# Kernel optimization log

Hardware: AMD Instinct MI355X
Metric: run time of the kernel (lower is better)

## Reference

```python
import jax, jax.numpy as jnp
import numpy as np
from jax import lax

D_MODEL = 1024
D_STATE = 16
D_CONV = 4
EXPAND = 2
D_INNER = EXPAND * D_MODEL
LN_EPS = 1e-5


def setup_inputs() -> dict:
    key = jax.random.key(0)
    ks = jax.random.split(key, 12)
    B, L = 4, 1024
    s = lambda fan_in: 1.0 / np.sqrt(fan_in)
    inp = {
        "x": jax.random.normal(ks[0], (B, L, D_MODEL), jnp.float32),
        # in_proj: d_model -> 2*d_inner (stored as (in, out))
        "W_in": jax.random.normal(ks[1], (D_MODEL, 2 * D_INNER), jnp.float32) * s(D_MODEL),
        "b_in": jnp.zeros((2 * D_INNER,), jnp.float32),
        # depthwise causal conv1d, kernel (d_inner, 1, d_conv)
        "conv_w": jax.random.normal(ks[2], (D_INNER, 1, D_CONV), jnp.float32) * s(D_CONV),
        "conv_b": jnp.zeros((D_INNER,), jnp.float32),
        # x_proj: d_inner -> 2*d_state
        "W_xp": jax.random.normal(ks[3], (D_INNER, 2 * D_STATE), jnp.float32) * s(D_INNER),
        "b_xp": jnp.zeros((2 * D_STATE,), jnp.float32),
        # dt_proj: d_inner -> d_inner
        "W_dt": jax.random.normal(ks[4], (D_INNER, D_INNER), jnp.float32) * s(D_INNER),
        "b_dt": jnp.zeros((D_INNER,), jnp.float32),
        # A_log = log(arange(1, d_state+1)) repeated over d_inner
        "A_log": jnp.log(jnp.broadcast_to(jnp.arange(1, D_STATE + 1, dtype=jnp.float32), (D_INNER, D_STATE))),
        "D_param": jnp.ones((D_INNER,), jnp.float32),
        # out_proj: d_inner -> d_model
        "W_out": jax.random.normal(ks[5], (D_INNER, D_MODEL), jnp.float32) * s(D_INNER),
        "b_out": jnp.zeros((D_MODEL,), jnp.float32),
        "ln_g": jnp.ones((D_MODEL,), jnp.float32),
        "ln_b": jnp.zeros((D_MODEL,), jnp.float32),
    }
    return inp


def _causal_depthwise_conv(x, w, b):
    # x: (B, d_inner, L); w: (d_inner, 1, d_conv). Left-pad d_conv-1 => causal.
    y = lax.conv_general_dilated(
        x, w, window_strides=(1,), padding=[(D_CONV - 1, 0)],
        dimension_numbers=("NCH", "OIH", "NCH"), feature_group_count=D_INNER)
    return y + b[None, :, None]


def _ssm(x, A, Bm, Cm, dt, D_param):
    # x, dt: (B,L,D)  A: (D,N)  Bm, Cm: (B,L,N)
    A_disc = jnp.exp(dt[..., None] * A)               # (B,L,D,N)
    dBx = (dt * x)[..., None] * Bm[:, :, None, :]     # (B,L,D,N) = dt*B*x_t
    h0 = jnp.zeros(x.shape[:1] + A.shape, x.dtype)    # (B,D,N)

    def step(h, inputs):
        a, bx, c = inputs                              # (B,D,N),(B,D,N),(B,N)
        h = a * h + bx
        y = jnp.einsum("bdn,bn->bd", h, c)
        return h, y

    _, ys = lax.scan(step, h0, (jnp.swapaxes(A_disc, 0, 1),
                                jnp.swapaxes(dBx, 0, 1),
                                jnp.swapaxes(Cm, 0, 1)))
    y = jnp.swapaxes(ys, 0, 1)                         # (B,L,D)
    return y + x * D_param


def reference(x, W_in, b_in, conv_w, conv_b, W_xp, b_xp, W_dt, b_dt,
              A_log, D_param, W_out, b_out, ln_g, ln_b):
    residual = x
    xr = x @ W_in + b_in                               # (B,L,2*d_inner)
    xi, res = jnp.split(xr, 2, axis=-1)
    xi = jax.nn.silu(xi)
    xi = jnp.swapaxes(xi, 1, 2)                        # (B,d_inner,L)
    xi = _causal_depthwise_conv(xi, conv_w, conv_b)
    xi = jnp.swapaxes(xi, 1, 2)
    xi = jax.nn.silu(xi)
    bc = xi @ W_xp + b_xp                              # (B,L,2*d_state)
    Bm, Cm = jnp.split(bc, 2, axis=-1)
    dt = jax.nn.softplus(xi @ W_dt + b_dt)
    A = -jnp.exp(A_log)                                # (d_inner, d_state)
    y = _ssm(xi, A, Bm, Cm, dt, D_param)
    y = y * jax.nn.silu(res)
    out = y @ W_out + b_out
    z = out + residual
    mu = jnp.mean(z, axis=-1, keepdims=True)
    var = jnp.var(z, axis=-1, keepdims=True)
    return (z - mu) * jax.lax.rsqrt(var + LN_EPS) * ln_g + ln_b
```

## Files before the change

### kernel.cpp

```cpp
#include <hip/hip_runtime.h>
#include <math.h>

#define D_MODEL 1024
#define D_INNER 2048
#define D_STATE 16
#define D_CONV  4
#define NCHUNK  8
#define LCHUNK  128

typedef unsigned short u16;
typedef __attribute__((ext_vector_type(8))) short short8;
typedef __attribute__((ext_vector_type(4))) float f32x4;
typedef __attribute__((ext_vector_type(4))) unsigned short u16x4;

__device__ __forceinline__ float silu_f(float x) { return x / (1.f + __expf(-x)); }
__device__ __forceinline__ float softplus_f(float x) {
    return fmaxf(x, 0.f) + log1pf(__expf(-fabsf(x)));
}
__device__ __forceinline__ u16 f2bf(float f) {
    union { float f; unsigned u; } c; c.f = f;
    unsigned r = c.u + 0x7fffu + ((c.u >> 16) & 1u);
    return (u16)(r >> 16);
}
__device__ __forceinline__ void gload_lds16(const void* g, void* l) {
    __builtin_amdgcn_global_load_lds((const __attribute__((address_space(1))) void*)g,
                                     (__attribute__((address_space(3))) void*)l, 16, 0, 0);
}

__global__ __launch_bounds__(256)
void f32_to_bf16_kernel(const float* __restrict__ in, u16* __restrict__ out, int n4)
{
    const int i = blockIdx.x * 256 + threadIdx.x;
    if (i >= n4) return;
    const float4 v = *(const float4*)&in[(size_t)i * 4];
    u16x4 o; o.x = f2bf(v.x); o.y = f2bf(v.y); o.z = f2bf(v.z); o.w = f2bf(v.w);
    *(u16x4*)&out[(size_t)i * 4] = o;
}

__global__ __launch_bounds__(256)
void transpose_bf16_kernel(const float* __restrict__ W, u16* __restrict__ Wt, int K, int N)
{
    __shared__ float tile[32][33];
    const int tx = threadIdx.x & 31, ty = threadIdx.x >> 5;
    const int n0 = blockIdx.x * 32, k0 = blockIdx.y * 32;
#pragma unroll
    for (int q = 0; q < 4; q++)
        tile[ty + q * 8][tx] = W[(size_t)(k0 + ty + q * 8) * N + n0 + tx];
    __syncthreads();
#pragma unroll
    for (int q = 0; q < 4; q++)
        Wt[(size_t)(n0 + ty + q * 8) * K + k0 + tx] = f2bf(tile[tx][ty + q * 8]);
}

template <int MODE>
__global__ __launch_bounds__(256)
void gemm_mfma(const u16* __restrict__ A, const u16* __restrict__ Bt,
               const float* __restrict__ bias, const float* __restrict__ aux,
               float* __restrict__ out0, float* __restrict__ out1,
               int M, int N, int K)
{
    __shared__ __align__(16) short As[2][4096];
    __shared__ __align__(16) short Bs[2][4096];

    const int tid = threadIdx.x;
    const int wid = tid >> 6, lane = tid & 63;
    const int wr = wid >> 1, wc = wid & 1;
    const int row0 = blockIdx.y * 128, col0 = blockIdx.x * 128;

    f32x4 acc[4][4] = {};

    const int c0 = wid * 128 + lane;
    const int c1 = c0 + 64;
    const u16* Abase = A + (size_t)row0 * K;
    const u16* Bbase = Bt + (size_t)col0 * K;

    const int gsl8 = (((lane & 3) ^ ((lane >> 3) & 3)) << 3);

    const int kg = lane >> 4, r16 = lane & 15;
    const int sl8 = ((kg ^ ((r16 >> 1) & 3)) << 3);

#define STAGE(bi, kk) do {                                                          \
        gload_lds16(Abase + (size_t)(c0 >> 2) * K + (kk) + gsl8, &As[bi][wid * 1024]);       \
        gload_lds16(Abase + (size_t)(c1 >> 2) * K + (kk) + gsl8, &As[bi][wid * 1024 + 512]); \
        gload_lds16(Bbase + (size_t)(c0 >> 2) * K + (kk) + gsl8, &Bs[bi][wid * 1024]);       \
        gload_lds16(Bbase + (size_t)(c1 >> 2) * K + (kk) + gsl8, &Bs[bi][wid * 1024 + 512]); \
    } while (0)

    const int nt = K >> 5;
    STAGE(0, 0);
    int cur = 0;
    for (int t = 0; t < nt; ++t) {
        if (t + 1 < nt) {
            STAGE(cur ^ 1, (t + 1) << 5);
            asm volatile("s_waitcnt vmcnt(4)" ::: "memory");
        } else {
            asm volatile("s_waitcnt vmcnt(0)" ::: "memory");
        }
        __builtin_amdgcn_s_barrier();

        short8 af[4], bg[4];
#pragma unroll
        for (int i = 0; i < 4; i++) {
            const int r = wr * 64 + i * 16 + r16;
            af[i] = *(const short8*)&As[cur][r * 32 + sl8];
        }
#pragma unroll
        for (int j = 0; j < 4; j++) {
            const int r = wc * 64 + j * 16 + r16;
            bg[j] = *(const short8*)&Bs[cur][r * 32 + sl8];
        }
#pragma unroll
        for (int i = 0; i < 4; i++)
#pragma unroll
            for (int j = 0; j < 4; j++)
                acc[i][j] = __builtin_amdgcn_mfma_f32_16x16x32_bf16(af[i], bg[j], acc[i][j], 0, 0, 0);

        asm volatile("s_waitcnt lgkmcnt(0)" ::: "memory");
        __builtin_amdgcn_s_barrier();
        cur ^= 1;
    }
#undef STAGE

#pragma unroll
    for (int i = 0; i < 4; i++) {
#pragma unroll
        for (int j = 0; j < 4; j++) {
#pragma unroll
            for (int r = 0; r < 4; r++) {
                const int row = row0 + wr * 64 + i * 16 + kg * 4 + r;
                const int col = col0 + wc * 64 + j * 16 + r16;
                float v = acc[i][j][r] + bias[col];
                if (MODE == 0) {
                    if (col < D_INNER) out0[(size_t)row * D_INNER + col] = silu_f(v);
                    else               out1[(size_t)row * D_INNER + (col - D_INNER)] = v;
                } else if (MODE == 1) {
                    out0[(size_t)row * N + col] = softplus_f(v);
                } else {
                    out0[(size_t)row * N + col] = v + aux[(size_t)row * N + col];
                }
            }
        }
    }
}

__global__ __launch_bounds__(256)
void conv_silu_kernel(const float* __restrict__ xi, const float* __restrict__ w,
                      const float* __restrict__ cb, float* __restrict__ xc,
                      u16* __restrict__ xcb, int total)
{
    const int i = blockIdx.x * 256 + threadIdx.x;
    if (i >= total) return;
    const int d = i & (D_INNER - 1);
    const int bl = i >> 11;
    const int l = bl & 1023;
    float acc = cb[d];
#pragma unroll
    for (int k = 0; k < D_CONV; k++) {
        const int li = l + k - (D_CONV - 1);
        if (li >= 0) acc = fmaf(w[d * D_CONV + k], xi[(size_t)i + (k - (D_CONV - 1)) * D_INNER], acc);
    }
    const float s = silu_f(acc);
    xc[i] = s;
    xcb[i] = f2bf(s);
}

__global__ __launch_bounds__(128)
void xproj_kernel(const float* __restrict__ xc, const float* __restrict__ W,
                  const float* __restrict__ bxp, float* __restrict__ bc)
{
    const int row = blockIdx.x;
    const int c = threadIdx.x & 31, s = threadIdx.x >> 5;
    const float* xr = xc + (size_t)row * D_INNER;
    float acc = 0.f;
    for (int k = s * 512; k < (s + 1) * 512; k += 4) {
        const float4 xv = *(const float4*)&xr[k];
        acc = fmaf(xv.x, W[(k + 0) * 32 + c], acc);
        acc = fmaf(xv.y, W[(k + 1) * 32 + c], acc);
        acc = fmaf(xv.z, W[(k + 2) * 32 + c], acc);
        acc = fmaf(xv.w, W[(k + 3) * 32 + c], acc);
    }
    __shared__ float red[4][32];
    red[s][c] = acc;
    __syncthreads();
    if (s == 0)
        bc[(size_t)row * 32 + c] = red[0][c] + red[1][c] + red[2][c] + red[3][c] + bxp[c];
}

__global__ __launch_bounds__(256)
void ssm_s1_kernel(const float* __restrict__ xc, const float* __restrict__ dt,
                   const float* __restrict__ bc, const float* __restrict__ A_log,
                   float* __restrict__ hend, float* __restrict__ dtsum)
{
    const int tid = threadIdx.x;
    const int ch = tid >> 4, n = tid & 15;
    const int d0 = blockIdx.x * 16;
    const int c = blockIdx.y;
    const int b = blockIdx.z;
    const int d = d0 + ch;

    const float Aln = -__expf(A_log[d * D_STATE + n]);

    __shared__ float sdt[64][16], sdtx[64][16], sB[64][16];

    float h = 0.f, S = 0.f;

    for (int half = 0; half < 2; half++) {
        const int l0 = c * LCHUNK + half * 64;
        __syncthreads();
        {
            const int l = tid >> 2, di = (tid & 3) << 2;
            const size_t g = ((size_t)(b * 1024 + l0 + l)) * D_INNER + d0 + di;
            const float4 dv = *(const float4*)&dt[g];
            const float4 xv = *(const float4*)&xc[g];
            float4 dx;
            dx.x = dv.x * xv.x; dx.y = dv.y * xv.y; dx.z = dv.z * xv.z; dx.w = dv.w * xv.w;
            *(float4*)&sdt[l][di] = dv;
            *(float4*)&sdtx[l][di] = dx;
            *(float4*)&sB[l][di] = *(const float4*)&bc[((size_t)(b * 1024 + l0 + l)) * 32 + di];
        }
        __syncthreads();
#pragma unroll 16
        for (int l = 0; l < 64; l++) {
            const float dtv = sdt[l][ch];
            const float a = __expf(dtv * Aln);
            h = fmaf(a, h, sdtx[l][ch] * sB[l][n]);
            S += dtv;
        }
    }
    hend[((size_t)(b * NCHUNK + c) * D_INNER + d) * D_STATE + n] = h;
    if (n == 0) dtsum[(size_t)(b * NCHUNK + c) * D_INNER + d] = S;
}

__global__ __launch_bounds__(256)
void ssm_s3_kernel(const float* __restrict__ xc, const float* __restrict__ dt,
                   const float* __restrict__ bc, const float* __restrict__ A_log,
                   const float* __restrict__ Dp, const float* __restrict__ res,
                   const float* __restrict__ hend, const float* __restrict__ dtsum,
                   u16* __restrict__ ybf)
{
    const int tid = threadIdx.x;
    const int wid = tid >> 6, lane = tid & 63;
    const int ch4 = lane >> 4, n = lane & 15;
    const int ch = wid * 4 + ch4;
    const int d0 = blockIdx.x * 16;
    const int c = blockIdx.y;
    const int b = blockIdx.z;
    const int d = d0 + ch;

    const float Aln = -__expf(A_log[d * D_STATE + n]);
    const float Dv = Dp[d];

    float h = 0.f;
    for (int cc = 0; cc < c; cc++) {
        const float S = dtsum[(size_t)(b * NCHUNK + cc) * D_INNER + d];
        const float P = __expf(Aln * S);
        h = fmaf(P, h, hend[((size_t)(b * NCHUNK + cc) * D_INNER + d) * D_STATE + n]);
    }

    __shared__ float sdt[64][16], sdtx[64][16], sx[64][16], sres[64][16];
    __shared__ float sbc[64][32];
    __shared__ float pbuf[4 * 16 * 68];

    float* pw = &pbuf[wid * 16 * 68];

    for (int half = 0; half < 2; half++) {
        const int l0 = c * LCHUNK + half * 64;
        __syncthreads();
        {
            const int l = tid >> 2, di = (tid & 3) << 2;
            const size_t g = ((size_t)(b * 1024 + l0 + l)) * D_INNER + d0 + di;
            const float4 dv = *(const float4*)&dt[g];
            const float4 xv = *(const float4*)&xc[g];
            const float4 rv = *(const float4*)&res[g];
            float4 dx;
            dx.x = dv.x * xv.x; dx.y = dv.y * xv.y; dx.z = dv.z * xv.z; dx.w = dv.w * xv.w;
            *(float4*)&sdt[l][di] = dv;
            *(float4*)&sdtx[l][di] = dx;
            *(float4*)&sx[l][di] = xv;
            *(float4*)&sres[l][di] = rv;
            const int r0 = tid >> 3, c4 = (tid & 7) << 2;
            *(float4*)&sbc[r0][c4] = *(const float4*)&bc[((size_t)(b * 1024 + l0 + r0)) * 32 + c4];
            const int r1 = (tid + 256) >> 3;
            *(float4*)&sbc[r1][c4] = *(const float4*)&bc[((size_t)(b * 1024 + l0 + r1)) * 32 + c4];
        }
        __syncthreads();

        for (int l16 = 0; l16 < 4; l16++) {
#pragma unroll
            for (int j = 0; j < 16; j++) {
                const int l = l16 * 16 + j;
                const float dtv = sdt[l][ch];
                const float a = __expf(dtv * Aln);
                h = fmaf(a, h, sdtx[l][ch] * sbc[l][n]);
                pw[j * 68 + ch4 * 16 + n] = h * sbc[l][16 + n];
            }
            __builtin_amdgcn_wave_barrier();
            const float4 q0 = *(const float4*)&pw[n * 68 + ch4 * 16 + 0];
            const float4 q1 = *(const float4*)&pw[n * 68 + ch4 * 16 + 4];
            const float4 q2 = *(const float4*)&pw[n * 68 + ch4 * 16 + 8];
            const float4 q3 = *(const float4*)&pw[n * 68 + ch4 * 16 + 12];
            const float sum = ((q0.x + q0.y) + (q0.z + q0.w)) + ((q1.x + q1.y) + (q1.z + q1.w))
                            + ((q2.x + q2.y) + (q2.z + q2.w)) + ((q3.x + q3.y) + (q3.z + q3.w));
            const int t = l16 * 16 + n;
            const float xv = sx[t][ch];
            const float rv = sres[t][ch];
            const float yv = (sum + xv * Dv) * silu_f(rv);
            ybf[((size_t)(b * 1024 + l0 + t)) * D_INNER + d] = f2bf(yv);
            __builtin_amdgcn_wave_barrier();
        }
    }
}

__global__ __launch_bounds__(256)
void layernorm_kernel(const float* __restrict__ z, const float* __restrict__ g,
                      const float* __restrict__ beta, float* __restrict__ out)
{
    const int row = blockIdx.x;
    const int tid = threadIdx.x;
    const float* zr = z + (size_t)row * D_MODEL;
    const float4 v = *(const float4*)&zr[tid << 2];
    float s = v.x + v.y + v.z + v.w;
    float ss = v.x * v.x + v.y * v.y + v.z * v.z + v.w * v.w;

    __shared__ float sm[256], sq[256];
    sm[tid] = s; sq[tid] = ss;
    __syncthreads();
    for (int off = 128; off > 0; off >>= 1) {
        if (tid < off) { sm[tid] += sm[tid + off]; sq[tid] += sq[tid + off]; }
        __syncthreads();
    }
    const float mean = sm[0] * (1.f / D_MODEL);
    const float var = sq[0] * (1.f / D_MODEL) - mean * mean;
    const float rstd = rsqrtf(var + 1e-5f);

    float4 o;
    o.x = (v.x - mean) * rstd * g[(tid << 2) + 0] + beta[(tid << 2) + 0];
    o.y = (v.y - mean) * rstd * g[(tid << 2) + 1] + beta[(tid << 2) + 1];
    o.z = (v.z - mean) * rstd * g[(tid << 2) + 2] + beta[(tid << 2) + 2];
    o.w = (v.w - mean) * rstd * g[(tid << 2) + 3] + beta[(tid << 2) + 3];
    *(float4*)&out[(size_t)row * D_MODEL + (tid << 2)] = o;
}

extern "C" void kernel_launch(void* const* d_in, const int* in_sizes, int n_in,
                              void* d_out, int out_size, void* d_ws, size_t ws_size,
                              hipStream_t stream)
{
    const float* x      = (const float*)d_in[0];
    const float* W_in   = (const float*)d_in[1];
    const float* b_in   = (const float*)d_in[2];
    const float* conv_w = (const float*)d_in[3];
    const float* conv_b = (const float*)d_in[4];
    const float* W_xp   = (const float*)d_in[5];
    const float* b_xp   = (const float*)d_in[6];
    const float* W_dt   = (const float*)d_in[7];
    const float* b_dt   = (const float*)d_in[8];
    const float* A_log  = (const float*)d_in[9];
    const float* D_par  = (const float*)d_in[10];
    const float* W_out  = (const float*)d_in[11];
    const float* b_out  = (const float*)d_in[12];
    const float* ln_g   = (const float*)d_in[13];
    const float* ln_b   = (const float*)d_in[14];
    float* out = (float*)d_out;

    const int BL = in_sizes[0] / D_MODEL;
    const int Bb = BL / 1024;
    const size_t BLD = (size_t)BL * D_INNER;

    float* ws = (float*)d_ws;
    float* xi_act = ws;
    float* resb   = ws + BLD;
    float* xcb    = ws + 2 * BLD;
    float* dtb    = ws + 3 * BLD;
    float* bcbuf  = ws + 4 * BLD;
    u16*   xbf    = (u16*)(ws + 4 * BLD + (size_t)BL * 32);
    u16*   xcbf   = xbf + (size_t)BL * D_MODEL;
    u16*   wtmp   = xcbf + BLD;
    float* hend   = (float*)(wtmp + (size_t)4 * 1024 * 1024);
    float* dtsum  = hend + (size_t)Bb * NCHUNK * D_INNER * D_STATE;
    u16*   ybf    = (u16*)xi_act;
    float* zbuf   = dtb;

    f32_to_bf16_kernel<<<(BL * D_MODEL / 4 + 255) / 256, 256, 0, stream>>>(x, xbf, BL * D_MODEL / 4);

    transpose_bf16_kernel<<<dim3(2 * D_INNER / 32, D_MODEL / 32), 256, 0, stream>>>(W_in, wtmp, D_MODEL, 2 * D_INNER);

    gemm_mfma<0><<<dim3(2 * D_INNER / 128, BL / 128), 256, 0, stream>>>(
        xbf, wtmp, b_in, nullptr, xi_act, resb, BL, 2 * D_INNER, D_MODEL);

    conv_silu_kernel<<<(int)(BLD / 256), 256, 0, stream>>>(
        xi_act, conv_w, conv_b, xcb, xcbf, (int)BLD);

    xproj_kernel<<<BL, 128, 0, stream>>>(xcb, W_xp, b_xp, bcbuf);

    transpose_bf16_kernel<<<dim3(D_INNER / 32, D_INNER / 32), 256, 0, stream>>>(W_dt, wtmp, D_INNER, D_INNER);

    gemm_mfma<1><<<dim3(D_INNER / 128, BL / 128), 256, 0, stream>>>(
        xcbf, wtmp, b_dt, nullptr, dtb, nullptr, BL, D_INNER, D_INNER);

    ssm_s1_kernel<<<dim3(D_INNER / 16, NCHUNK, Bb), 256, 0, stream>>>(
        xcb, dtb, bcbuf, A_log, hend, dtsum);

    ssm_s3_kernel<<<dim3(D_INNER / 16, NCHUNK, Bb), 256, 0, stream>>>(
        xcb, dtb, bcbuf, A_log, D_par, resb, hend, dtsum, ybf);

    transpose_bf16_kernel<<<dim3(D_MODEL / 32, D_INNER / 32), 256, 0, stream>>>(W_out, wtmp, D_INNER, D_MODEL);

    gemm_mfma<2><<<dim3(D_MODEL / 128, BL / 128), 256, 0, stream>>>(
        ybf, wtmp, b_out, x, zbuf, nullptr, BL, D_MODEL, D_INNER);

    layernorm_kernel<<<BL, 256, 0, stream>>>(zbuf, ln_g, ln_b, out);
}
```

Baseline: 403.4 us.

## Triple-buffer GEMM, store in_proj outputs as bf16, MFMA x_proj

The GEMM main loop moves from double to triple buffering of the LDS tiles, with two stages in flight and raised wave priority around the MFMA block. The in_proj GEMM now writes its silu and residual halves as bf16, which halves that write traffic and the later reads in the conv and SSM kernels. The scalar fp32 x_proj kernel is replaced by an MFMA kernel that reads the bf16 conv output and a transposed bf16 W_xp. This adds bf16 rounding on the pre-conv activations, the gate branch and the B/C projection, and uses more LDS per GEMM block, which can reduce occupancy.

```diff
diff --git a/kernel.cpp b/kernel.cpp
--- a/kernel.cpp
+++ b/kernel.cpp
@@ -22,6 +22,9 @@
     unsigned r = c.u + 0x7fffu + ((c.u >> 16) & 1u);
     return (u16)(r >> 16);
 }
+__device__ __forceinline__ float bf2f(u16 v) {
+    union { unsigned u; float f; } c; c.u = ((unsigned)v) << 16; return c.f;
+}
 __device__ __forceinline__ void gload_lds16(const void* g, void* l) {
     __builtin_amdgcn_global_load_lds((const __attribute__((address_space(1))) void*)g,
                                      (__attribute__((address_space(3))) void*)l, 16, 0, 0);
@@ -56,11 +59,11 @@
 __global__ __launch_bounds__(256)
 void gemm_mfma(const u16* __restrict__ A, const u16* __restrict__ Bt,
                const float* __restrict__ bias, const float* __restrict__ aux,
-               float* __restrict__ out0, float* __restrict__ out1,
+               void* __restrict__ out0v, void* __restrict__ out1v,
                int M, int N, int K)
 {
-    __shared__ __align__(16) short As[2][4096];
-    __shared__ __align__(16) short Bs[2][4096];
+    __shared__ __align__(16) short As[3][4096];
+    __shared__ __align__(16) short Bs[3][4096];
 
     const int tid = threadIdx.x;
     const int wid = tid >> 6, lane = tid & 63;
@@ -79,7 +82,7 @@
     const int kg = lane >> 4, r16 = lane & 15;
     const int sl8 = ((kg ^ ((r16 >> 1) & 3)) << 3);
 
-#define STAGE(bi, kk) do {                                                          \
+#define STAGE(bi, kk) do {                                                                   \
         gload_lds16(Abase + (size_t)(c0 >> 2) * K + (kk) + gsl8, &As[bi][wid * 1024]);       \
         gload_lds16(Abase + (size_t)(c1 >> 2) * K + (kk) + gsl8, &As[bi][wid * 1024 + 512]); \
         gload_lds16(Bbase + (size_t)(c0 >> 2) * K + (kk) + gsl8, &Bs[bi][wid * 1024]);       \
@@ -88,10 +91,14 @@
 
     const int nt = K >> 5;
     STAGE(0, 0);
-    int cur = 0;
+    STAGE(1, 32);
+    int cs = 0;
     for (int t = 0; t < nt; ++t) {
-        if (t + 1 < nt) {
-            STAGE(cur ^ 1, (t + 1) << 5);
+        if (t + 2 < nt) {
+            const int ss = (cs + 2 >= 3) ? cs - 1 : cs + 2;
+            STAGE(ss, (t + 2) << 5);
+            asm volatile("s_waitcnt vmcnt(8)" ::: "memory");
+        } else if (t + 1 < nt) {
             asm volatile("s_waitcnt vmcnt(4)" ::: "memory");
         } else {
             asm volatile("s_waitcnt vmcnt(0)" ::: "memory");
@@ -102,22 +109,24 @@
 #pragma unroll
         for (int i = 0; i < 4; i++) {
             const int r = wr * 64 + i * 16 + r16;
-            af[i] = *(const short8*)&As[cur][r * 32 + sl8];
+            af[i] = *(const short8*)&As[cs][r * 32 + sl8];
         }
 #pragma unroll
         for (int j = 0; j < 4; j++) {
             const int r = wc * 64 + j * 16 + r16;
-            bg[j] = *(const short8*)&Bs[cur][r * 32 + sl8];
-        }
+            bg[j] = *(const short8*)&Bs[cs][r * 32 + sl8];
+        }
+        __builtin_amdgcn_s_setprio(1);
 #pragma unroll
         for (int i = 0; i < 4; i++)
 #pragma unroll
             for (int j = 0; j < 4; j++)
                 acc[i][j] = __builtin_amdgcn_mfma_f32_16x16x32_bf16(af[i], bg[j], acc[i][j], 0, 0, 0);
+        __builtin_amdgcn_s_setprio(0);
 
         asm volatile("s_waitcnt lgkmcnt(0)" ::: "memory");
         __builtin_amdgcn_s_barrier();
-        cur ^= 1;
+        cs = (cs + 1 >= 3) ? 0 : cs + 1;
     }
 #undef STAGE
 
@@ -131,12 +140,13 @@
                 const int col = col0 + wc * 64 + j * 16 + r16;
                 float v = acc[i][j][r] + bias[col];
                 if (MODE == 0) {
-                    if (col < D_INNER) out0[(size_t)row * D_INNER + col] = silu_f(v);
-                    else               out1[(size_t)row * D_INNER + (col - D_INNER)] = v;
+                    u16* o0 = (u16*)out0v; u16* o1 = (u16*)out1v;
+                    if (col < D_INNER) o0[(size_t)row * D_INNER + col] = f2bf(silu_f(v));
+                    else               o1[(size_t)row * D_INNER + (col - D_INNER)] = f2bf(v);
                 } else if (MODE == 1) {
-                    out0[(size_t)row * N + col] = softplus_f(v);
+                    ((float*)out0v)[(size_t)row * N + col] = softplus_f(v);
                 } else {
-                    out0[(size_t)row * N + col] = v + aux[(size_t)row * N + col];
+                    ((float*)out0v)[(size_t)row * N + col] = v + aux[(size_t)row * N + col];
                 }
             }
         }
@@ -144,46 +154,50 @@
 }
 
 __global__ __launch_bounds__(256)
-void conv_silu_kernel(const float* __restrict__ xi, const float* __restrict__ w,
+void conv_silu_kernel(const u16* __restrict__ xi, const float* __restrict__ w,
                       const float* __restrict__ cb, float* __restrict__ xc,
                       u16* __restrict__ xcb, int total)
 {
     const int i = blockIdx.x * 256 + threadIdx.x;
     if (i >= total) return;
     const int d = i & (D_INNER - 1);
-    const int bl = i >> 11;
-    const int l = bl & 1023;
+    const int l = (i >> 11) & 1023;
     float acc = cb[d];
 #pragma unroll
     for (int k = 0; k < D_CONV; k++) {
         const int li = l + k - (D_CONV - 1);
-        if (li >= 0) acc = fmaf(w[d * D_CONV + k], xi[(size_t)i + (k - (D_CONV - 1)) * D_INNER], acc);
+        if (li >= 0) acc = fmaf(w[d * D_CONV + k], bf2f(xi[(size_t)i + (k - (D_CONV - 1)) * D_INNER]), acc);
     }
     const float s = silu_f(acc);
     xc[i] = s;
     xcb[i] = f2bf(s);
 }
 
-__global__ __launch_bounds__(128)
-void xproj_kernel(const float* __restrict__ xc, const float* __restrict__ W,
-                  const float* __restrict__ bxp, float* __restrict__ bc)
-{
-    const int row = blockIdx.x;
-    const int c = threadIdx.x & 31, s = threadIdx.x >> 5;
-    const float* xr = xc + (size_t)row * D_INNER;
-    float acc = 0.f;
-    for (int k = s * 512; k < (s + 1) * 512; k += 4) {
-        const float4 xv = *(const float4*)&xr[k];
-        acc = fmaf(xv.x, W[(k + 0) * 32 + c], acc);
-        acc = fmaf(xv.y, W[(k + 1) * 32 + c], acc);
-        acc = fmaf(xv.z, W[(k + 2) * 32 + c], acc);
-        acc = fmaf(xv.w, W[(k + 3) * 32 + c], acc);
-    }
-    __shared__ float red[4][32];
-    red[s][c] = acc;
-    __syncthreads();
-    if (s == 0)
-        bc[(size_t)row * 32 + c] = red[0][c] + red[1][c] + red[2][c] + red[3][c] + bxp[c];
+__global__ __launch_bounds__(256)
+void xproj_mfma_kernel(const u16* __restrict__ A, const u16* __restrict__ Wt,
+                       const float* __restrict__ bxp, float* __restrict__ bc)
+{
+    const int wid = threadIdx.x >> 6, lane = threadIdx.x & 63;
+    const int kg = lane >> 4, r16 = lane & 15;
+    const int tok0 = blockIdx.x * 64 + wid * 16;
+
+    f32x4 acc[2] = {};
+#pragma unroll 4
+    for (int k0 = 0; k0 < D_INNER; k0 += 32) {
+        const short8 a  = *(const short8*)&A[(size_t)(tok0 + r16) * D_INNER + k0 + kg * 8];
+        const short8 b0 = *(const short8*)&Wt[(size_t)r16 * D_INNER + k0 + kg * 8];
+        const short8 b1 = *(const short8*)&Wt[(size_t)(16 + r16) * D_INNER + k0 + kg * 8];
+        acc[0] = __builtin_amdgcn_mfma_f32_16x16x32_bf16(a, b0, acc[0], 0, 0, 0);
+        acc[1] = __builtin_amdgcn_mfma_f32_16x16x32_bf16(a, b1, acc[1], 0, 0, 0);
+    }
+#pragma unroll
+    for (int j = 0; j < 2; j++)
+#pragma unroll
+        for (int r = 0; r < 4; r++) {
+            const int token = tok0 + kg * 4 + r;
+            const int c = j * 16 + r16;
+            bc[(size_t)token * 32 + c] = acc[j][r] + bxp[c];
+        }
 }
 
 __global__ __launch_bounds__(256)
@@ -234,7 +248,7 @@
 __global__ __launch_bounds__(256)
 void ssm_s3_kernel(const float* __restrict__ xc, const float* __restrict__ dt,
                    const float* __restrict__ bc, const float* __restrict__ A_log,
-                   const float* __restrict__ Dp, const float* __restrict__ res,
+                   const float* __restrict__ Dp, const u16* __restrict__ resbf,
                    const float* __restrict__ hend, const float* __restrict__ dtsum,
                    u16* __restrict__ ybf)
 {
@@ -271,13 +285,16 @@
             const size_t g = ((size_t)(b * 1024 + l0 + l)) * D_INNER + d0 + di;
             const float4 dv = *(const float4*)&dt[g];
             const float4 xv = *(const float4*)&xc[g];
-            const float4 rv = *(const float4*)&res[g];
+            const u16x4 rv = *(const u16x4*)&resbf[g];
             float4 dx;
             dx.x = dv.x * xv.x; dx.y = dv.y * xv.y; dx.z = dv.z * xv.z; dx.w = dv.w * xv.w;
             *(float4*)&sdt[l][di] = dv;
             *(float4*)&sdtx[l][di] = dx;
             *(float4*)&sx[l][di] = xv;
-            *(float4*)&sres[l][di] = rv;
+            sres[l][di + 0] = bf2f(rv.x);
+            sres[l][di + 1] = bf2f(rv.y);
+            sres[l][di + 2] = bf2f(rv.z);
+            sres[l][di + 3] = bf2f(rv.w);
             const int r0 = tid >> 3, c4 = (tid & 7) << 2;
             *(float4*)&sbc[r0][c4] = *(const float4*)&bc[((size_t)(b * 1024 + l0 + r0)) * 32 + c4];
             const int r1 = (tid + 256) >> 3;
@@ -366,31 +383,34 @@
     const int Bb = BL / 1024;
     const size_t BLD = (size_t)BL * D_INNER;
 
-    float* ws = (float*)d_ws;
-    float* xi_act = ws;
-    float* resb   = ws + BLD;
-    float* xcb    = ws + 2 * BLD;
-    float* dtb    = ws + 3 * BLD;
-    float* bcbuf  = ws + 4 * BLD;
-    u16*   xbf    = (u16*)(ws + 4 * BLD + (size_t)BL * 32);
-    u16*   xcbf   = xbf + (size_t)BL * D_MODEL;
-    u16*   wtmp   = xcbf + BLD;
-    float* hend   = (float*)(wtmp + (size_t)4 * 1024 * 1024);
-    float* dtsum  = hend + (size_t)Bb * NCHUNK * D_INNER * D_STATE;
-    u16*   ybf    = (u16*)xi_act;
-    float* zbuf   = dtb;
+    float* ws    = (float*)d_ws;
+    float* xcb   = ws;
+    float* dtb   = xcb + BLD;
+    float* bcbuf = dtb + BLD;
+    float* hend  = bcbuf + (size_t)BL * 32;
+    float* dtsum = hend + (size_t)Bb * NCHUNK * D_INNER * D_STATE;
+    u16*   xibf  = (u16*)(dtsum + (size_t)Bb * NCHUNK * D_INNER);
+    u16*   resbf = xibf + BLD;
+    u16*   xcbf  = resbf + BLD;
+    u16*   xbf   = xcbf + BLD;
+    u16*   wxpT  = xbf + (size_t)BL * D_MODEL;
+    u16*   wtmp  = wxpT + 32 * D_INNER;
+    u16*   ybf   = xibf;
+    float* zbuf  = dtb;
 
     f32_to_bf16_kernel<<<(BL * D_MODEL / 4 + 255) / 256, 256, 0, stream>>>(x, xbf, BL * D_MODEL / 4);
 
     transpose_bf16_kernel<<<dim3(2 * D_INNER / 32, D_MODEL / 32), 256, 0, stream>>>(W_in, wtmp, D_MODEL, 2 * D_INNER);
 
     gemm_mfma<0><<<dim3(2 * D_INNER / 128, BL / 128), 256, 0, stream>>>(
-        xbf, wtmp, b_in, nullptr, xi_act, resb, BL, 2 * D_INNER, D_MODEL);
+        xbf, wtmp, b_in, nullptr, xibf, resbf, BL, 2 * D_INNER, D_MODEL);
+
+    transpose_bf16_kernel<<<dim3(1, D_INNER / 32), 256, 0, stream>>>(W_xp, wxpT, D_INNER, 32);
 
     conv_silu_kernel<<<(int)(BLD / 256), 256, 0, stream>>>(
-        xi_act, conv_w, conv_b, xcb, xcbf, (int)BLD);
-
-    xproj_kernel<<<BL, 128, 0, stream>>>(xcb, W_xp, b_xp, bcbuf);
+        xibf, conv_w, conv_b, xcb, xcbf, (int)BLD);
+
+    xproj_mfma_kernel<<<BL / 64, 256, 0, stream>>>(xcbf, wxpT, b_xp, bcbuf);
 
     transpose_bf16_kernel<<<dim3(D_INNER / 32, D_INNER / 32), 256, 0, stream>>>(W_dt, wtmp, D_INNER, D_INNER);
 
@@ -401,7 +421,7 @@
         xcb, dtb, bcbuf, A_log, hend, dtsum);
 
     ssm_s3_kernel<<<dim3(D_INNER / 16, NCHUNK, Bb), 256, 0, stream>>>(
-        xcb, dtb, bcbuf, A_log, D_par, resb, hend, dtsum, ybf);
+        xcb, dtb, bcbuf, A_log, D_par, resbf, hend, dtsum, ybf);
 
     transpose_bf16_kernel<<<dim3(D_MODEL / 32, D_INNER / 32), 256, 0, stream>>>(W_out, wtmp, D_INNER, D_MODEL);
 
```

New measurement: 368.2 us. 1.1x faster.
